# Optimization experiments

Measured on AMD Instinct MI355X. Metric: run time of the kernel, lower is better.

## Reference

```python
import jax, jax.numpy as jnp
import numpy as np

IN_SIZE = 4096
OUT_SIZE = 4096
NUM_ROWS = 256
NUM_COLS = 256
IN_BLOCKS = 16   # ceil(4096/256)
OUT_BLOCKS = 16
BATCH = 128
QUANTIZE = 'log'
QUANTIZE_BITS = 8
G_INF = 2.0
G_MIN = 0.001
TAU = 0.75


def rram_quantize(w, tau, g_inf, g_min, bits, mode):
    """Snap each element of w to the nearest of 2**bits RRAM conductance levels.
    mode='log': saturating-exponential pulse model; mode='linear': uniform levels.
    Vectorized over the whole array (equivalent to the original per-element vmap).
    """
    L = 2 ** bits
    n = jnp.arange(L, dtype=w.dtype)
    if mode == 'log':
        scale = (g_inf - g_min) / (1.0 - jnp.exp(jnp.asarray(-tau, w.dtype)))
        levels = g_min + scale * (1.0 - jnp.exp(-tau * n / (L - 1)))
    else:
        levels = g_min + (g_inf - g_min) * n / (L - 1)
    # levels is monotonically increasing -> nearest-level via searchsorted
    idx = jnp.clip(jnp.searchsorted(levels, w), 1, L - 1)
    lo = levels[idx - 1]
    hi = levels[idx]
    return jnp.where(w - lo < hi - w, lo, hi)


def setup_inputs() -> dict:
    key = jax.random.key(0)
    kx, kc = jax.random.split(key)
    x = jax.random.normal(kx, (BATCH, IN_SIZE), dtype=jnp.float32)
    # glorot_normal over last two dims (fan_in=num_cols, fan_out=num_rows)
    std = float(np.sqrt(2.0 / (NUM_ROWS + NUM_COLS)))
    cores = std * jax.random.normal(kc, (OUT_BLOCKS, IN_BLOCKS, NUM_ROWS, NUM_COLS), dtype=jnp.float32)
    return {'x': x, 'cores': cores}


def reference(x, cores):
    # pad input to in_blocks * num_rows and split into blocks
    pad = NUM_ROWS * IN_BLOCKS - IN_SIZE  # = 0 here, kept for faithfulness
    x_padded = jnp.pad(x, ((0, 0), (0, pad)))
    x_blocks = x_padded.reshape(x.shape[0], IN_BLOCKS, NUM_ROWS)  # (b, j, l)
    # relu then RRAM quantization of the cores
    w = jax.nn.relu(cores)
    w = rram_quantize(w, TAU, G_INF, G_MIN, QUANTIZE_BITS, QUANTIZE)
    # blockwise batched matmul: (i,j,k,l),(b,j,l)->(b,i,j,k)
    y = jnp.einsum('ijkl,bjl->bijk', w, x_blocks)
    return y
```

## Files before the change

### kernel.cpp

```cpp
#include <hip/hip_runtime.h>
#include <hip/hip_bf16.h>
#include <math.h>


typedef __attribute__((ext_vector_type(4))) float f32x4;
typedef __attribute__((ext_vector_type(8))) short bf16x8;
typedef __attribute__((ext_vector_type(8))) short s16x8;
typedef __attribute__((ext_vector_type(4))) short s16x4;

#define TAU   0.75f
#define G_INF 2.0f
#define G_MIN 0.001f

__device__ __forceinline__ short f2bf_rne(float f) {
    union { float f; unsigned u; } v; v.f = f;
    unsigned u = v.u;
    return (short)((u + 0x7FFFu + ((u >> 16) & 1u)) >> 16);
}

__global__ __launch_bounds__(256)
void xcvt(const float* __restrict__ xin, short* __restrict__ xbf) {
    int idx = (blockIdx.x * 256 + threadIdx.x) * 8;
    f32x4 a = *(const f32x4*)(xin + idx);
    f32x4 b = *(const f32x4*)(xin + idx + 4);
    s16x8 o;
    o[0] = f2bf_rne(a[0]); o[1] = f2bf_rne(a[1]);
    o[2] = f2bf_rne(a[2]); o[3] = f2bf_rne(a[3]);
    o[4] = f2bf_rne(b[0]); o[5] = f2bf_rne(b[1]);
    o[6] = f2bf_rne(b[2]); o[7] = f2bf_rne(b[3]);
    *(s16x8*)(xbf + idx) = o;
}

template<bool XBF>
__global__ __launch_bounds__(256, 8)
void bd_fused(const float* __restrict__ x,
              const short* __restrict__ xbf,
              const float* __restrict__ cores,
              float* __restrict__ out)
{
    __shared__ unsigned char wq[32 * 512];

    const int tid  = threadIdx.x;
    const int wave = tid >> 6;
    const int lane = tid & 63;
    const int l15  = lane & 15;
    const int l4   = lane >> 4;

    const int bid = blockIdx.x;
    const int ns  = bid & 7;
    const int j   = (bid >> 3) & 15;
    const int i   = bid >> 7;
    const int k0  = ns * 32;

    const float scale     = (G_INF - G_MIN) / (1.0f - expf(-TAU));
    const float inv_scale = 1.0f / scale;
    const float kn = -(255.0f / TAU) * 0.69314718055994531f;
    const float c2 = -(TAU / 255.0f) * 1.44269504088896341f;
    const float Ac = G_MIN + scale;
    const float Bc = scale * (1.0f - expf(-TAU / 255.0f));

    const float* wsrc = cores + (((size_t)(i * 16 + j)) << 16) + ((size_t)k0 << 8);
    #pragma unroll
    for (int it = 0; it < 8; ++it) {
        int e = it * 1024 + tid * 4;
        f32x4 v = *(const f32x4*)(wsrc + e);
        s16x4 q;
        #pragma unroll
        for (int c = 0; c < 4; ++c) {
            float w = fmaxf(v[c], 0.0f);
            float t = 1.0f - (w - G_MIN) * inv_scale;
            t = fmaxf(t, 1e-8f);
            float nr = kn * __log2f(t);
            int f = (int)floorf(nr);
            f = f < 0 ? 0 : (f > 254 ? 254 : f);
            float ef = exp2f(c2 * (float)f);
            float lo = Ac - scale * ef;
            float hi = lo + Bc * ef;
            float qv = (w - lo < hi - w) ? lo : hi;
            q[c] = f2bf_rne(qv);
        }
        int r   = e >> 8;
        int kb  = (e & 255) * 2;
        int off = (r * 512 + kb) ^ ((r & 7) << 4);
        *(s16x4*)(wq + off) = q;
    }
    __syncthreads();

    const int brow0 = wave * 32;

    f32x4 acc[2][2];
    #pragma unroll
    for (int nt = 0; nt < 2; ++nt)
        #pragma unroll
        for (int mt = 0; mt < 2; ++mt)
            acc[nt][mt] = (f32x4){0.f, 0.f, 0.f, 0.f};

    const short* xb = xbf + (size_t)(brow0 + l15) * 4096 + j * 256 + l4 * 8;
    const float* xf = x   + (size_t)(brow0 + l15) * 4096 + j * 256 + l4 * 8;

    #pragma unroll
    for (int s = 0; s < 8; ++s) {
        bf16x8 bfr[2];
        #pragma unroll
        for (int mt = 0; mt < 2; ++mt) {
            if (XBF) {
                bfr[mt] = *(const bf16x8*)(xb + (size_t)mt * 65536 + s * 32);
            } else {
                const float* p = xf + (size_t)mt * 65536 + s * 32;
                f32x4 v0 = *(const f32x4*)p;
                f32x4 v1 = *(const f32x4*)(p + 4);
                bf16x8 b;
                b[0] = f2bf_rne(v0[0]); b[1] = f2bf_rne(v0[1]);
                b[2] = f2bf_rne(v0[2]); b[3] = f2bf_rne(v0[3]);
                b[4] = f2bf_rne(v1[0]); b[5] = f2bf_rne(v1[1]);
                b[6] = f2bf_rne(v1[2]); b[7] = f2bf_rne(v1[3]);
                bfr[mt] = b;
            }
        }
        #pragma unroll
        for (int nt = 0; nt < 2; ++nt) {
            int r   = nt * 16 + l15;
            int off = (r * 512 + s * 64 + l4 * 16) ^ ((r & 7) << 4);
            bf16x8 afr = *(const bf16x8*)(wq + off);
            acc[nt][0] = __builtin_amdgcn_mfma_f32_16x16x32_bf16(afr, bfr[0], acc[nt][0], 0, 0, 0);
            acc[nt][1] = __builtin_amdgcn_mfma_f32_16x16x32_bf16(afr, bfr[1], acc[nt][1], 0, 0, 0);
        }
    }

    #pragma unroll
    for (int nt = 0; nt < 2; ++nt) {
        #pragma unroll
        for (int mt = 0; mt < 2; ++mt) {
            int b  = brow0 + mt * 16 + l15;
            int kg = k0 + nt * 16 + (l4 << 2);
            *(f32x4*)(out + (((size_t)((b * 16 + i) * 16 + j)) << 8) + kg) = acc[nt][mt];
        }
    }
}

extern "C" void kernel_launch(void* const* d_in, const int* in_sizes, int n_in,
                              void* d_out, int out_size, void* d_ws, size_t ws_size,
                              hipStream_t stream) {
    const float* x     = (const float*)d_in[0];
    const float* cores = (const float*)d_in[1];
    float* out = (float*)d_out;

    const size_t xbytes = (size_t)128 * 4096 * sizeof(short);
    if (ws_size >= xbytes) {
        short* xbf = (short*)d_ws;
        xcvt<<<dim3(256), dim3(256), 0, stream>>>(x, xbf);
        bd_fused<true><<<dim3(2048), dim3(256), 0, stream>>>(x, xbf, cores, out);
    } else {
        bd_fused<false><<<dim3(2048), dim3(256), 0, stream>>>(x, nullptr, cores, out);
    }
}
```

Measured before the change: 37.21 us.

## Halve k-tile per block, prefetch x into registers, simplify log-quantize rounding

Each block now covers 16 output rows instead of 32, so the grid doubles to 4096 blocks and LDS per block halves. All x fragments and the weight vectors are loaded into registers up front, so the global x loads overlap with the quantization math instead of following the barrier. The nearest-level selection is rewritten as a closed-form rounding threshold on the fractional level index, which removes the lo/hi comparison. In exchange, x is re-read twice as often across blocks, the register footprint grows (launch bounds relaxed to 4), and the new threshold rounding may differ from the reference near ties.

Result: slower. 46.12 us (+23.9%).

```diff
diff --git a/kernel.cpp b/kernel.cpp
--- a/kernel.cpp
+++ b/kernel.cpp
@@ -18,6 +18,8 @@
     return (short)((u + 0x7FFFu + ((u >> 16) & 1u)) >> 16);
 }
 
+__device__ __forceinline__ void pin4(f32x4& v) { asm volatile("" : "+v"(v)); }
+
 __global__ __launch_bounds__(256)
 void xcvt(const float* __restrict__ xin, short* __restrict__ xbf) {
     int idx = (blockIdx.x * 256 + threadIdx.x) * 8;
@@ -32,13 +34,13 @@
 }
 
 template<bool XBF>
-__global__ __launch_bounds__(256, 8)
+__global__ __launch_bounds__(256, 4)
 void bd_fused(const float* __restrict__ x,
               const short* __restrict__ xbf,
               const float* __restrict__ cores,
               float* __restrict__ out)
 {
-    __shared__ unsigned char wq[32 * 512];
+    __shared__ unsigned char wq[16 * 512];
 
     const int tid  = threadIdx.x;
     const int wave = tid >> 6;
@@ -47,64 +49,36 @@
     const int l4   = lane >> 4;
 
     const int bid = blockIdx.x;
-    const int ns  = bid & 7;
-    const int j   = (bid >> 3) & 15;
-    const int i   = bid >> 7;
-    const int k0  = ns * 32;
+    const int ns  = bid & 15;
+    const int j   = (bid >> 4) & 15;
+    const int i   = bid >> 8;
+    const int k0  = ns * 16;
 
     const float scale     = (G_INF - G_MIN) / (1.0f - expf(-TAU));
     const float inv_scale = 1.0f / scale;
+    const float T0 = 1.0f + G_MIN * inv_scale;
     const float kn = -(255.0f / TAU) * 0.69314718055994531f;
     const float c2 = -(TAU / 255.0f) * 1.44269504088896341f;
     const float Ac = G_MIN + scale;
-    const float Bc = scale * (1.0f - expf(-TAU / 255.0f));
+    const float rho = expf(-TAU / 255.0f);
+    const float Cf  = logf((1.0f + rho) * 0.5f) / logf(rho);
 
     const float* wsrc = cores + (((size_t)(i * 16 + j)) << 16) + ((size_t)k0 << 8);
+    f32x4 wv[4];
     #pragma unroll
-    for (int it = 0; it < 8; ++it) {
-        int e = it * 1024 + tid * 4;
-        f32x4 v = *(const f32x4*)(wsrc + e);
-        s16x4 q;
-        #pragma unroll
-        for (int c = 0; c < 4; ++c) {
-            float w = fmaxf(v[c], 0.0f);
-            float t = 1.0f - (w - G_MIN) * inv_scale;
-            t = fmaxf(t, 1e-8f);
-            float nr = kn * __log2f(t);
-            int f = (int)floorf(nr);
-            f = f < 0 ? 0 : (f > 254 ? 254 : f);
-            float ef = exp2f(c2 * (float)f);
-            float lo = Ac - scale * ef;
-            float hi = lo + Bc * ef;
-            float qv = (w - lo < hi - w) ? lo : hi;
-            q[c] = f2bf_rne(qv);
-        }
-        int r   = e >> 8;
-        int kb  = (e & 255) * 2;
-        int off = (r * 512 + kb) ^ ((r & 7) << 4);
-        *(s16x4*)(wq + off) = q;
-    }
-    __syncthreads();
+    for (int it = 0; it < 4; ++it)
+        wv[it] = *(const f32x4*)(wsrc + it * 1024 + tid * 4);
 
     const int brow0 = wave * 32;
-
-    f32x4 acc[2][2];
-    #pragma unroll
-    for (int nt = 0; nt < 2; ++nt)
-        #pragma unroll
-        for (int mt = 0; mt < 2; ++mt)
-            acc[nt][mt] = (f32x4){0.f, 0.f, 0.f, 0.f};
-
     const short* xb = xbf + (size_t)(brow0 + l15) * 4096 + j * 256 + l4 * 8;
     const float* xf = x   + (size_t)(brow0 + l15) * 4096 + j * 256 + l4 * 8;
-
+    bf16x8 bfr[8][2];
     #pragma unroll
     for (int s = 0; s < 8; ++s) {
-        bf16x8 bfr[2];
         #pragma unroll
         for (int mt = 0; mt < 2; ++mt) {
             if (XBF) {
-                bfr[mt] = *(const bf16x8*)(xb + (size_t)mt * 65536 + s * 32);
+                bfr[s][mt] = *(const bf16x8*)(xb + (size_t)mt * 65536 + s * 32);
             } else {
                 const float* p = xf + (size_t)mt * 65536 + s * 32;
                 f32x4 v0 = *(const f32x4*)p;
@@ -114,27 +88,58 @@
                 b[2] = f2bf_rne(v0[2]); b[3] = f2bf_rne(v0[3]);
                 b[4] = f2bf_rne(v1[0]); b[5] = f2bf_rne(v1[1]);
                 b[6] = f2bf_rne(v1[2]); b[7] = f2bf_rne(v1[3]);
-                bfr[mt] = b;
+                bfr[s][mt] = b;
             }
-        }
-        #pragma unroll
-        for (int nt = 0; nt < 2; ++nt) {
-            int r   = nt * 16 + l15;
-            int off = (r * 512 + s * 64 + l4 * 16) ^ ((r & 7) << 4);
-            bf16x8 afr = *(const bf16x8*)(wq + off);
-            acc[nt][0] = __builtin_amdgcn_mfma_f32_16x16x32_bf16(afr, bfr[0], acc[nt][0], 0, 0, 0);
-            acc[nt][1] = __builtin_amdgcn_mfma_f32_16x16x32_bf16(afr, bfr[1], acc[nt][1], 0, 0, 0);
         }
     }
 
     #pragma unroll
-    for (int nt = 0; nt < 2; ++nt) {
+    for (int it = 0; it < 4; ++it) {
+        s16x4 q;
         #pragma unroll
-        for (int mt = 0; mt < 2; ++mt) {
-            int b  = brow0 + mt * 16 + l15;
-            int kg = k0 + nt * 16 + (l4 << 2);
-            *(f32x4*)(out + (((size_t)((b * 16 + i) * 16 + j)) << 8) + kg) = acc[nt][mt];
+        for (int c = 0; c < 4; ++c) {
+            float w = fmaxf(wv[it][c], 0.0f);
+            float t = fmaf(w, -inv_scale, T0);
+            t = fmaxf(t, 1e-8f);
+            float nr = kn * __log2f(t);
+            nr = fminf(fmaxf(nr, 0.0f), 255.0f);
+            float ff = floorf(nr);
+            float g  = (nr - ff < Cf) ? ff : ff + 1.0f;
+            float ef = exp2f(c2 * g);
+            float qv = fmaf(ef, -scale, Ac);
+            q[c] = f2bf_rne(qv);
         }
+        int e   = it * 1024 + tid * 4;
+        int r   = e >> 8;
+        int kb  = (e & 255) * 2;
+        int off = (r * 512 + kb) ^ ((r & 7) << 4);
+        *(s16x4*)(wq + off) = q;
+    }
+    __syncthreads();
+
+    #pragma unroll
+    for (int s = 0; s < 8; ++s) {
+        pin4(*(f32x4*)&bfr[s][0]);
+        pin4(*(f32x4*)&bfr[s][1]);
+    }
+
+    f32x4 acc[2];
+    acc[0] = (f32x4){0.f, 0.f, 0.f, 0.f};
+    acc[1] = (f32x4){0.f, 0.f, 0.f, 0.f};
+
+    #pragma unroll
+    for (int s = 0; s < 8; ++s) {
+        int off = (l15 * 512 + s * 64 + l4 * 16) ^ ((l15 & 7) << 4);
+        bf16x8 afr = *(const bf16x8*)(wq + off);
+        acc[0] = __builtin_amdgcn_mfma_f32_16x16x32_bf16(afr, bfr[s][0], acc[0], 0, 0, 0);
+        acc[1] = __builtin_amdgcn_mfma_f32_16x16x32_bf16(afr, bfr[s][1], acc[1], 0, 0, 0);
+    }
+
+    #pragma unroll
+    for (int mt = 0; mt < 2; ++mt) {
+        int b  = brow0 + mt * 16 + l15;
+        int kg = k0 + (l4 << 2);
+        *(f32x4*)(out + (((size_t)((b * 16 + i) * 16 + j)) << 8) + kg) = acc[mt];
     }
 }
 
@@ -149,8 +154,8 @@
     if (ws_size >= xbytes) {
         short* xbf = (short*)d_ws;
         xcvt<<<dim3(256), dim3(256), 0, stream>>>(x, xbf);
-        bd_fused<true><<<dim3(2048), dim3(256), 0, stream>>>(x, xbf, cores, out);
+        bd_fused<true><<<dim3(4096), dim3(256), 0, stream>>>(x, xbf, cores, out);
     } else {
-        bd_fused<false><<<dim3(2048), dim3(256), 0, stream>>>(x, nullptr, cores, out);
+        bd_fused<false><<<dim3(4096), dim3(256), 0, stream>>>(x, nullptr, cores, out);
     }
 }
```

## Stream raw fp32 cores into LDS asynchronously and quantize at fragment load

Applied to the files above, without the earlier changes.

Each block now owns one (i,j) core and walks all eight 32-row k-slices. Raw fp32 weights are double-buffered into LDS with global_load_lds, so the next slice loads while the current one computes. Quantization moves to fragment-load time using a simplified nearest-level formula (a floor with a precomputed offset instead of comparing lo and hi). x fragments are loaded once per block and reused across slices. The grid drops from 2048 to 256 blocks at one block per CU, which risks lower occupancy and less latency hiding, and the new rounding could differ from the reference at level boundaries.

Measured after the change: 61.43 us. 1.65x slower.

```diff
diff --git a/kernel.cpp b/kernel.cpp
--- a/kernel.cpp
+++ b/kernel.cpp
@@ -6,7 +6,6 @@
 typedef __attribute__((ext_vector_type(4))) float f32x4;
 typedef __attribute__((ext_vector_type(8))) short bf16x8;
 typedef __attribute__((ext_vector_type(8))) short s16x8;
-typedef __attribute__((ext_vector_type(4))) short s16x4;
 
 #define TAU   0.75f
 #define G_INF 2.0f
@@ -16,6 +15,13 @@
     union { float f; unsigned u; } v; v.f = f;
     unsigned u = v.u;
     return (short)((u + 0x7FFFu + ((u >> 16) & 1u)) >> 16);
+}
+
+__device__ __forceinline__ void gll16(const void* g, void* l) {
+    typedef const unsigned int __attribute__((address_space(1)))* gp1;
+    typedef unsigned int __attribute__((address_space(3)))* lp3;
+    __builtin_amdgcn_global_load_lds((gp1)(const unsigned int*)g,
+                                     (lp3)(unsigned int*)l, 16, 0, 0);
 }
 
 __global__ __launch_bounds__(256)
@@ -32,13 +38,13 @@
 }
 
 template<bool XBF>
-__global__ __launch_bounds__(256, 8)
+__global__ __launch_bounds__(256, 1)
 void bd_fused(const float* __restrict__ x,
               const short* __restrict__ xbf,
               const float* __restrict__ cores,
               float* __restrict__ out)
 {
-    __shared__ unsigned char wq[32 * 512];
+    __shared__ unsigned char wraw[2][32768];
 
     const int tid  = threadIdx.x;
     const int wave = tid >> 6;
@@ -47,93 +53,108 @@
     const int l4   = lane >> 4;
 
     const int bid = blockIdx.x;
-    const int ns  = bid & 7;
-    const int j   = (bid >> 3) & 15;
-    const int i   = bid >> 7;
-    const int k0  = ns * 32;
+    const int j   = bid & 15;
+    const int i   = bid >> 4;
 
     const float scale     = (G_INF - G_MIN) / (1.0f - expf(-TAU));
     const float inv_scale = 1.0f / scale;
+    const float T0 = 1.0f + G_MIN * inv_scale;
     const float kn = -(255.0f / TAU) * 0.69314718055994531f;
     const float c2 = -(TAU / 255.0f) * 1.44269504088896341f;
     const float Ac = G_MIN + scale;
-    const float Bc = scale * (1.0f - expf(-TAU / 255.0f));
+    const float rho = expf(-TAU / 255.0f);
+    const float Df  = 1.0f - logf((1.0f + rho) * 0.5f) / logf(rho);
 
-    const float* wsrc = cores + (((size_t)(i * 16 + j)) << 16) + ((size_t)k0 << 8);
-    #pragma unroll
-    for (int it = 0; it < 8; ++it) {
-        int e = it * 1024 + tid * 4;
-        f32x4 v = *(const f32x4*)(wsrc + e);
-        s16x4 q;
+    const unsigned char* wblk =
+        (const unsigned char*)(cores + (((size_t)(i * 16 + j)) << 16));
+
+    auto STAGE = [&](int t, int b) {
         #pragma unroll
-        for (int c = 0; c < 4; ++c) {
-            float w = fmaxf(v[c], 0.0f);
-            float t = 1.0f - (w - G_MIN) * inv_scale;
-            t = fmaxf(t, 1e-8f);
-            float nr = kn * __log2f(t);
-            int f = (int)floorf(nr);
-            f = f < 0 ? 0 : (f > 254 ? 254 : f);
-            float ef = exp2f(c2 * (float)f);
-            float lo = Ac - scale * ef;
-            float hi = lo + Bc * ef;
-            float qv = (w - lo < hi - w) ? lo : hi;
-            q[c] = f2bf_rne(qv);
+        for (int n = 0; n < 8; ++n) {
+            int o   = n * 4096 + tid * 16;
+            int src = o ^ ((((unsigned)o >> 10) & 7) << 4);
+            gll16(wblk + (size_t)t * 32768 + src,
+                  &wraw[b][n * 4096 + wave * 1024]);
         }
-        int r   = e >> 8;
-        int kb  = (e & 255) * 2;
-        int off = (r * 512 + kb) ^ ((r & 7) << 4);
-        *(s16x4*)(wq + off) = q;
-    }
-    __syncthreads();
+    };
+
+    STAGE(0, 0);
+    STAGE(1, 1);
 
     const int brow0 = wave * 32;
-
-    f32x4 acc[2][2];
-    #pragma unroll
-    for (int nt = 0; nt < 2; ++nt)
-        #pragma unroll
-        for (int mt = 0; mt < 2; ++mt)
-            acc[nt][mt] = (f32x4){0.f, 0.f, 0.f, 0.f};
-
+    bf16x8 bfr[8][2];
     const short* xb = xbf + (size_t)(brow0 + l15) * 4096 + j * 256 + l4 * 8;
     const float* xf = x   + (size_t)(brow0 + l15) * 4096 + j * 256 + l4 * 8;
-
     #pragma unroll
     for (int s = 0; s < 8; ++s) {
-        bf16x8 bfr[2];
         #pragma unroll
         for (int mt = 0; mt < 2; ++mt) {
             if (XBF) {
-                bfr[mt] = *(const bf16x8*)(xb + (size_t)mt * 65536 + s * 32);
+                bfr[s][mt] = *(const bf16x8*)(xb + (size_t)mt * 65536 + s * 32);
             } else {
                 const float* p = xf + (size_t)mt * 65536 + s * 32;
                 f32x4 v0 = *(const f32x4*)p;
                 f32x4 v1 = *(const f32x4*)(p + 4);
-                bf16x8 b;
-                b[0] = f2bf_rne(v0[0]); b[1] = f2bf_rne(v0[1]);
-                b[2] = f2bf_rne(v0[2]); b[3] = f2bf_rne(v0[3]);
-                b[4] = f2bf_rne(v1[0]); b[5] = f2bf_rne(v1[1]);
-                b[6] = f2bf_rne(v1[2]); b[7] = f2bf_rne(v1[3]);
-                bfr[mt] = b;
+                bf16x8 bb;
+                bb[0] = f2bf_rne(v0[0]); bb[1] = f2bf_rne(v0[1]);
+                bb[2] = f2bf_rne(v0[2]); bb[3] = f2bf_rne(v0[3]);
+                bb[4] = f2bf_rne(v1[0]); bb[5] = f2bf_rne(v1[1]);
+                bb[6] = f2bf_rne(v1[2]); bb[7] = f2bf_rne(v1[3]);
+                bfr[s][mt] = bb;
             }
-        }
-        #pragma unroll
-        for (int nt = 0; nt < 2; ++nt) {
-            int r   = nt * 16 + l15;
-            int off = (r * 512 + s * 64 + l4 * 16) ^ ((r & 7) << 4);
-            bf16x8 afr = *(const bf16x8*)(wq + off);
-            acc[nt][0] = __builtin_amdgcn_mfma_f32_16x16x32_bf16(afr, bfr[0], acc[nt][0], 0, 0, 0);
-            acc[nt][1] = __builtin_amdgcn_mfma_f32_16x16x32_bf16(afr, bfr[1], acc[nt][1], 0, 0, 0);
         }
     }
 
-    #pragma unroll
-    for (int nt = 0; nt < 2; ++nt) {
+    __syncthreads();
+
+    for (int t = 0; t < 8; ++t) {
+        const unsigned char* buf = wraw[t & 1];
+
+        f32x4 acc[2][2];
         #pragma unroll
-        for (int mt = 0; mt < 2; ++mt) {
-            int b  = brow0 + mt * 16 + l15;
-            int kg = k0 + nt * 16 + (l4 << 2);
-            *(f32x4*)(out + (((size_t)((b * 16 + i) * 16 + j)) << 8) + kg) = acc[nt][mt];
+        for (int nt = 0; nt < 2; ++nt)
+            #pragma unroll
+            for (int mt = 0; mt < 2; ++mt)
+                acc[nt][mt] = (f32x4){0.f, 0.f, 0.f, 0.f};
+
+        #pragma unroll
+        for (int s = 0; s < 8; ++s) {
+            #pragma unroll
+            for (int nt = 0; nt < 2; ++nt) {
+                int r  = nt * 16 + l15;
+                int a  = r * 1024 + s * 128 + l4 * 32;
+                int sw = (r & 7) << 4;
+                f32x4 v0 = *(const f32x4*)(buf + ((a     ) ^ sw));
+                f32x4 v1 = *(const f32x4*)(buf + ((a + 16) ^ sw));
+                bf16x8 afr;
+                #pragma unroll
+                for (int e = 0; e < 8; ++e) {
+                    float w = fmaxf(e < 4 ? v0[e & 3] : v1[e & 3], 0.0f);
+                    float tt = fmaf(w, -inv_scale, T0);
+                    tt = fmaxf(tt, 1e-8f);
+                    float nr = kn * __log2f(tt);
+                    float g  = floorf(nr + Df);
+                    float qv = fmaf(exp2f(c2 * g), -scale, Ac);
+                    afr[e] = f2bf_rne(qv);
+                }
+                acc[nt][0] = __builtin_amdgcn_mfma_f32_16x16x32_bf16(afr, bfr[s][0], acc[nt][0], 0, 0, 0);
+                acc[nt][1] = __builtin_amdgcn_mfma_f32_16x16x32_bf16(afr, bfr[s][1], acc[nt][1], 0, 0, 0);
+            }
+        }
+
+        if (t < 7) {
+            __syncthreads();
+            if (t + 2 < 8) STAGE(t + 2, t & 1);
+        }
+
+        #pragma unroll
+        for (int nt = 0; nt < 2; ++nt) {
+            #pragma unroll
+            for (int mt = 0; mt < 2; ++mt) {
+                int b  = brow0 + mt * 16 + l15;
+                int kg = t * 32 + nt * 16 + (l4 << 2);
+                *(f32x4*)(out + (((size_t)((b * 16 + i) * 16 + j)) << 8) + kg) = acc[nt][mt];
+            }
         }
     }
 }
@@ -149,8 +170,8 @@
     if (ws_size >= xbytes) {
         short* xbf = (short*)d_ws;
         xcvt<<<dim3(256), dim3(256), 0, stream>>>(x, xbf);
-        bd_fused<true><<<dim3(2048), dim3(256), 0, stream>>>(x, xbf, cores, out);
+        bd_fused<true><<<dim3(256), dim3(256), 0, stream>>>(x, xbf, cores, out);
     } else {
-        bd_fused<false><<<dim3(2048), dim3(256), 0, stream>>>(x, nullptr, cores, out);
+        bd_fused<false><<<dim3(256), dim3(256), 0, stream>>>(x, nullptr, cores, out);
     }
 }
```
